# Optimization experiments

Hardware: AMD Instinct MI355X
Metric: run time of the kernel (lower is better)

Reference implementation:

```python
import jax, jax.numpy as jnp
from jax import lax
import numpy as np

VOCAB, EMB, HID = 6, 64, 64


def _glorot(key, shape):
    fan_in, fan_out = shape[0], shape[-1]
    lim = np.sqrt(6.0 / (fan_in + fan_out)).astype(np.float32)
    return jax.random.uniform(key, shape, jnp.float32, -lim, lim)


def setup_inputs() -> dict:
    key = jax.random.key(0)
    ks = jax.random.split(key, 10)
    B, T = 256, 2048
    tokens = jax.random.randint(ks[0], (B, T), 0, VOCAB, dtype=jnp.int32)
    emb = jax.random.normal(ks[1], (VOCAB, EMB), jnp.float32) * 0.05  # Keras uniform init approx
    # LSTM kernels: gate order i, f, c(g), o ; kernel [EMB,4H], recurrent [H,4H], bias [4H]
    W_f = _glorot(ks[2], (EMB, 4 * HID))
    U_f = _glorot(ks[3], (HID, 4 * HID))
    b_f = jnp.zeros((4 * HID,), jnp.float32).at[HID:2 * HID].set(1.0)  # unit_forget_bias
    W_b = _glorot(ks[4], (EMB, 4 * HID))
    U_b = _glorot(ks[5], (HID, 4 * HID))
    b_b = jnp.zeros((4 * HID,), jnp.float32).at[HID:2 * HID].set(1.0)
    W_d = _glorot(ks[6], (2 * HID, 1))
    b_d = jnp.zeros((1,), jnp.float32)
    return {"tokens": tokens, "emb": emb, "W_f": W_f, "U_f": U_f, "b_f": b_f,
            "W_b": W_b, "U_b": U_b, "b_b": b_b, "W_d": W_d, "b_d": b_d}


def _masked_lstm(x, mask, W, U, b):
    """x: [B,T,E] float, mask: [B,T] bool. Returns [B,T,H].
    Keras mask semantics: at masked steps, state AND output carry previous values."""
    B = x.shape[0]
    h0 = jnp.zeros((B, HID), x.dtype)
    c0 = jnp.zeros((B, HID), x.dtype)

    def step(carry, inp):
        h, c = carry
        xt, mt = inp  # [B,E], [B]
        z = xt @ W + h @ U + b  # [B,4H]
        i, f, g, o = jnp.split(z, 4, axis=-1)
        c_new = jax.nn.sigmoid(f) * c + jax.nn.sigmoid(i) * jnp.tanh(g)
        h_new = jax.nn.sigmoid(o) * jnp.tanh(c_new)
        m = mt[:, None]
        h2 = jnp.where(m, h_new, h)
        c2 = jnp.where(m, c_new, c)
        return (h2, c2), h2

    xs = (jnp.swapaxes(x, 0, 1), jnp.swapaxes(mask, 0, 1))  # time-major
    _, hs = lax.scan(step, (h0, c0), xs)
    return jnp.swapaxes(hs, 0, 1)  # [B,T,H]


def reference(tokens, emb, W_f, U_f, b_f, W_b, U_b, b_b, W_d, b_d):
    mask = tokens != 0  # mask_zero=True
    x = emb[tokens]  # [B,T,EMB]
    fwd = _masked_lstm(x, mask, W_f, U_f, b_f)
    # backward direction: reverse inputs and mask in time, run, reverse outputs back
    bwd = _masked_lstm(x[:, ::-1], mask[:, ::-1], W_b, U_b, b_b)[:, ::-1]
    seq = jnp.concatenate([fwd, bwd], axis=-1)  # [B,T,2H]
    last = seq[:, -1, :]
    return last @ W_d + b_d  # [B,1]
```

## Files before the change

kernel.cpp:

```cpp
#include <hip/hip_runtime.h>


#define TT 2048
#define L2E 1.4426950408889634f

__device__ __forceinline__ float fexp2(float x) { return __builtin_amdgcn_exp2f(x); }
__device__ __forceinline__ float frcp(float x)  { return __builtin_amdgcn_rcpf(x); }
__device__ __forceinline__ float fsigm(float x) { return frcp(1.f + fexp2(-L2E * x)); }
__device__ __forceinline__ float ftanh(float x) { return fmaf(2.f, frcp(1.f + fexp2(-2.f * L2E * x)), -1.f); }
__device__ __forceinline__ float readlane_f(float v, int l) {
  return __builtin_bit_cast(float, __builtin_amdgcn_readlane(__builtin_bit_cast(int, v), l));
}

__global__ __launch_bounds__(256) void lstm_fused(
    const int* __restrict__ tokens,
    const float* __restrict__ emb,
    const float* __restrict__ W_f, const float* __restrict__ U_f, const float* __restrict__ b_f,
    const float* __restrict__ W_b, const float* __restrict__ b_b,
    const float* __restrict__ W_d, const float* __restrict__ b_d,
    float* __restrict__ out)
{
  const int b    = blockIdx.x;
  const int tid  = threadIdx.x;
  const int lane = tid & 63;
  const int wv   = tid >> 6;
  const int g    = lane >> 4;
  const int ug   = lane & 15;

  __shared__ int   tok_s[TT + 8];
  __shared__ float emb_s[6 * 64];
  __shared__ float zx_s [6 * 288];
  __shared__ float zxb_s[6 * 256];
  __shared__ float part[2][4][288] __attribute__((aligned(16)));
  __shared__ float h_s[64];

  {
    const int4* tsrc = (const int4*)(tokens + b * TT);
    int4* tdst = (int4*)tok_s;
    for (int i = tid; i < TT / 4; i += 256) tdst[i] = tsrc[i];
    if (tid < 8) tok_s[TT + tid] = 0;
    for (int i = tid; i < 384; i += 256) emb_s[i] = emb[i];
  }
  __syncthreads();

  {
    float af[6], ab[6];
#pragma unroll
    for (int v = 0; v < 6; ++v) { af[v] = b_f[tid]; ab[v] = b_b[tid]; }
    for (int e = 0; e < 64; ++e) {
      const float wf = W_f[e * 256 + tid];
      const float wb = W_b[e * 256 + tid];
#pragma unroll
      for (int v = 0; v < 6; ++v) {
        af[v] = fmaf(emb_s[v * 64 + e], wf, af[v]);
        ab[v] = fmaf(emb_s[v * 64 + e], wb, ab[v]);
      }
    }
#pragma unroll
    for (int v = 0; v < 6; ++v) {
      zx_s [v * 288 + (tid >> 6) * 72 + (tid & 63)] = af[v];
      zxb_s[v * 256 + tid] = ab[v];
    }
  }

  float4 Uc[16];
#pragma unroll
  for (int r = 0; r < 16; ++r)
    Uc[r] = *(const float4*)&U_f[(16 * wv + r) * 256 + 64 * g + 4 * ug];

  __syncthreads();

  const int roff = g * 72 + 16 * wv + ug;
  const float m1 = (g == 2) ? (-2.f * L2E) : (-L2E);
  const float ya = (g == 2) ? 2.f : 1.f;
  const float yb = (g == 2) ? -1.f : 0.f;

  float h_reg = 0.f;
  float c_reg = 0.f;
  int   buf   = 0;
  int   tok   = __builtin_amdgcn_readfirstlane(tok_s[0]);

  for (int t = 0; t < TT; ++t) {
    const int tok_n = __builtin_amdgcn_readfirstlane(tok_s[t + 1]);
    if (tok != 0) {
      float p0 = 0.f, p1 = 0.f, p2 = 0.f, p3 = 0.f;
#pragma unroll
      for (int r = 0; r < 16; ++r) {
        const float hk = readlane_f(h_reg, r);
        p0 = fmaf(hk, Uc[r].x, p0);
        p1 = fmaf(hk, Uc[r].y, p1);
        p2 = fmaf(hk, Uc[r].z, p2);
        p3 = fmaf(hk, Uc[r].w, p3);
      }
      *(float4*)&part[buf][wv][g * 72 + 4 * ug] = float4{p0, p1, p2, p3};
      const float zxv = zx_s[tok * 288 + roff];
      __syncthreads();
      const float z = ((part[buf][0][roff] + part[buf][1][roff]) +
                       (part[buf][2][roff] + part[buf][3][roff])) + zxv;
      const float y = fmaf(ya, frcp(1.f + fexp2(z * m1)), yb);
      const float vf = __shfl(y, ug + 16, 64);
      const float vg = __shfl(y, ug + 32, 64);
      const float vo = __shfl(y, ug + 48, 64);
      c_reg = fmaf(vf, c_reg, y * vg);
      h_reg = vo * ftanh(c_reg);
      buf ^= 1;
    }
    tok = tok_n;
  }

  if (lane < 16) h_s[16 * wv + ug] = h_reg;
  __syncthreads();
  if (tid < 64) {
    const float hf   = h_s[tid];
    const int   tokL = tok_s[TT - 1];
    float hbv = 0.f;
    if (tokL != 0) {
      const float zi = zxb_s[tokL * 256 + tid];
      const float zg = zxb_s[tokL * 256 + 128 + tid];
      const float zo = zxb_s[tokL * 256 + 192 + tid];
      const float cn = fsigm(zi) * ftanh(zg);
      hbv = fsigm(zo) * ftanh(cn);
    }
    float pr = fmaf(hf, W_d[tid], hbv * W_d[64 + tid]);
#pragma unroll
    for (int off = 32; off > 0; off >>= 1) pr += __shfl_xor(pr, off, 64);
    if (tid == 0) out[b] = pr + b_d[0];
  }
}

extern "C" void kernel_launch(void* const* d_in, const int* in_sizes, int n_in,
                              void* d_out, int out_size, void* d_ws, size_t ws_size,
                              hipStream_t stream) {
  const int*   tokens = (const int*)d_in[0];
  const float* emb    = (const float*)d_in[1];
  const float* W_f    = (const float*)d_in[2];
  const float* U_f    = (const float*)d_in[3];
  const float* b_f    = (const float*)d_in[4];
  const float* W_b    = (const float*)d_in[5];
  const float* U_b    = (const float*)d_in[6];
  (void)U_b;
  const float* b_b    = (const float*)d_in[7];
  const float* W_d    = (const float*)d_in[8];
  const float* b_d    = (const float*)d_in[9];
  float* out = (float*)d_out;
  (void)d_ws; (void)ws_size;

  lstm_fused<<<256, 256, 0, stream>>>(tokens, emb, W_f, U_f, b_f, W_b, b_b,
                                      W_d, b_d, out);
}
```

Measured before the change: 807.8 us.

## Compact active tokens and compute full gate columns per wave

```diff
diff --git a/kernel.cpp b/kernel.cpp
--- a/kernel.cpp
+++ b/kernel.cpp
@@ -12,7 +12,7 @@
   return __builtin_bit_cast(float, __builtin_amdgcn_readlane(__builtin_bit_cast(int, v), l));
 }
 
-__global__ __launch_bounds__(256) void lstm_fused(
+__global__ __launch_bounds__(256, 1) void lstm_fused(
     const int* __restrict__ tokens,
     const float* __restrict__ emb,
     const float* __restrict__ W_f, const float* __restrict__ U_f, const float* __restrict__ b_f,
@@ -23,25 +23,48 @@
   const int b    = blockIdx.x;
   const int tid  = threadIdx.x;
   const int lane = tid & 63;
-  const int wv   = tid >> 6;
-  const int g    = lane >> 4;
-  const int ug   = lane & 15;
+  const int g    = tid >> 6;
 
-  __shared__ int   tok_s[TT + 8];
+  __shared__ int   tok_s [TT + 8];
+  __shared__ int   ctok_s[TT + 8];
   __shared__ float emb_s[6 * 64];
-  __shared__ float zx_s [6 * 288];
+  __shared__ float zx_s [6 * 272];
   __shared__ float zxb_s[6 * 256];
-  __shared__ float part[2][4][288] __attribute__((aligned(16)));
-  __shared__ float h_s[64];
+  __shared__ float act_s[2][4 * 68];
+  __shared__ int   wsum[4];
 
   {
     const int4* tsrc = (const int4*)(tokens + b * TT);
     int4* tdst = (int4*)tok_s;
     for (int i = tid; i < TT / 4; i += 256) tdst[i] = tsrc[i];
-    if (tid < 8) tok_s[TT + tid] = 0;
+    if (tid < 8) { tok_s[TT + tid] = 0; ctok_s[TT + tid] = 0; }
     for (int i = tid; i < 384; i += 256) emb_s[i] = emb[i];
   }
   __syncthreads();
+
+  int mytok[8];
+  int cnt = 0;
+#pragma unroll
+  for (int j = 0; j < 8; ++j) {
+    mytok[j] = tok_s[tid * 8 + j];
+    cnt += (mytok[j] != 0);
+  }
+  int inc = cnt;
+#pragma unroll
+  for (int off = 1; off < 64; off <<= 1) {
+    int v = __shfl_up(inc, off, 64);
+    if (lane >= off) inc += v;
+  }
+  if (lane == 63) wsum[g] = inc;
+  __syncthreads();
+  int base = 0;
+#pragma unroll
+  for (int w = 0; w < 4; ++w) base += (w < g) ? wsum[w] : 0;
+  int pos = base + inc - cnt;
+#pragma unroll
+  for (int j = 0; j < 8; ++j)
+    if (mytok[j] != 0) ctok_s[pos++] = mytok[j];
+  const int nact = __builtin_amdgcn_readfirstlane(wsum[0] + wsum[1] + wsum[2] + wsum[3]);
 
   {
     float af[6], ab[6];
@@ -58,60 +81,56 @@
     }
 #pragma unroll
     for (int v = 0; v < 6; ++v) {
-      zx_s [v * 288 + (tid >> 6) * 72 + (tid & 63)] = af[v];
+      zx_s [v * 272 + g * 68 + lane] = af[v];
       zxb_s[v * 256 + tid] = ab[v];
     }
   }
 
-  float4 Uc[16];
+  float Ucol[64];
 #pragma unroll
-  for (int r = 0; r < 16; ++r)
-    Uc[r] = *(const float4*)&U_f[(16 * wv + r) * 256 + 64 * g + 4 * ug];
+  for (int k = 0; k < 64; ++k) {
+    Ucol[k] = U_f[k * 256 + (g << 6) + lane];
+    asm volatile("" : "+v"(Ucol[k]));
+  }
 
   __syncthreads();
 
-  const int roff = g * 72 + 16 * wv + ug;
   const float m1 = (g == 2) ? (-2.f * L2E) : (-L2E);
   const float ya = (g == 2) ? 2.f : 1.f;
   const float yb = (g == 2) ? -1.f : 0.f;
+  const int   goff = g * 68 + lane;
 
-  float h_reg = 0.f;
-  float c_reg = 0.f;
-  int   buf   = 0;
-  int   tok   = __builtin_amdgcn_readfirstlane(tok_s[0]);
+  float h_reg = 0.f, c_reg = 0.f;
+  int   buf = 0;
+  int   tokc = ctok_s[0];
 
-  for (int t = 0; t < TT; ++t) {
-    const int tok_n = __builtin_amdgcn_readfirstlane(tok_s[t + 1]);
-    if (tok != 0) {
-      float p0 = 0.f, p1 = 0.f, p2 = 0.f, p3 = 0.f;
+  for (int s = 0; s < nact; ++s) {
+    const int tokn = ctok_s[s + 1];
+    const float zxv = zx_s[tokc * 272 + goff];
+    float a0 = 0.f, a1 = 0.f, a2 = 0.f, a3 = 0.f;
 #pragma unroll
-      for (int r = 0; r < 16; ++r) {
-        const float hk = readlane_f(h_reg, r);
-        p0 = fmaf(hk, Uc[r].x, p0);
-        p1 = fmaf(hk, Uc[r].y, p1);
-        p2 = fmaf(hk, Uc[r].z, p2);
-        p3 = fmaf(hk, Uc[r].w, p3);
-      }
-      *(float4*)&part[buf][wv][g * 72 + 4 * ug] = float4{p0, p1, p2, p3};
-      const float zxv = zx_s[tok * 288 + roff];
-      __syncthreads();
-      const float z = ((part[buf][0][roff] + part[buf][1][roff]) +
-                       (part[buf][2][roff] + part[buf][3][roff])) + zxv;
-      const float y = fmaf(ya, frcp(1.f + fexp2(z * m1)), yb);
-      const float vf = __shfl(y, ug + 16, 64);
-      const float vg = __shfl(y, ug + 32, 64);
-      const float vo = __shfl(y, ug + 48, 64);
-      c_reg = fmaf(vf, c_reg, y * vg);
-      h_reg = vo * ftanh(c_reg);
-      buf ^= 1;
+    for (int k = 0; k < 64; k += 4) {
+      a0 = fmaf(readlane_f(h_reg, k + 0), Ucol[k + 0], a0);
+      a1 = fmaf(readlane_f(h_reg, k + 1), Ucol[k + 1], a1);
+      a2 = fmaf(readlane_f(h_reg, k + 2), Ucol[k + 2], a2);
+      a3 = fmaf(readlane_f(h_reg, k + 3), Ucol[k + 3], a3);
     }
-    tok = tok_n;
+    const float z = zxv + ((a0 + a1) + (a2 + a3));
+    const float y = fmaf(ya, frcp(1.f + fexp2(z * m1)), yb);
+    act_s[buf][goff] = y;
+    __syncthreads();
+    const float ai  = act_s[buf][lane];
+    const float af2 = act_s[buf][68 + lane];
+    const float ag  = act_s[buf][136 + lane];
+    const float ao  = act_s[buf][204 + lane];
+    c_reg = fmaf(af2, c_reg, ai * ag);
+    h_reg = ao * ftanh(c_reg);
+    buf ^= 1;
+    tokc = tokn;
   }
 
-  if (lane < 16) h_s[16 * wv + ug] = h_reg;
-  __syncthreads();
   if (tid < 64) {
-    const float hf   = h_s[tid];
+    const float hf   = h_reg;
     const int   tokL = tok_s[TT - 1];
     float hbv = 0.f;
     if (tokL != 0) {
```

Result: faster. 740.7 us (-8.3%).
